# Kernel tuning notes

Measured on AMD Instinct MI355X. Metric: run time of the kernel, lower is better.

The kernel has to match this reference:

```python
import jax, jax.numpy as jnp
import numpy as np

IN, HID, B = 512, 512, 16384

def _linear_params(key, fan_in, fan_out, bias_const=None):
    kw, kb = jax.random.split(key)
    bound = 1.0 / np.sqrt(fan_in)
    W = jax.random.uniform(kw, (fan_out, fan_in), jnp.float32, -bound, bound)
    if bias_const is None:
        b = jax.random.uniform(kb, (fan_out,), jnp.float32, -bound, bound)
    else:
        b = jnp.full((fan_out,), bias_const, jnp.float32)
    return W, b

def setup_inputs() -> dict:
    key = jax.random.key(0)
    ks = jax.random.split(key, 11)
    x = jax.random.normal(ks[0], (B, IN), jnp.float32)
    h = jax.random.normal(ks[1], (B, HID), jnp.float32)
    c = jax.random.normal(ks[2], (B, HID), jnp.float32)
    Wxi, bxi = _linear_params(ks[3], IN, HID)
    Wxo, bxo = _linear_params(ks[4], IN, HID)
    Wxf, bxf = _linear_params(ks[5], IN, HID, bias_const=1.0)
    Wxg, bxg = _linear_params(ks[6], IN, HID)
    Whi, bhi = _linear_params(ks[7], HID, HID)
    Who, bho = _linear_params(ks[8], HID, HID)
    Whf, bhf = _linear_params(ks[9], HID, HID, bias_const=1.0)
    Whg, bhg = _linear_params(ks[10], HID, HID)
    return dict(x=x, h=h, c=c,
                Wxi=Wxi, bxi=bxi, Wxo=Wxo, bxo=bxo, Wxf=Wxf, bxf=bxf, Wxg=Wxg, bxg=bxg,
                Whi=Whi, bhi=bhi, Who=Who, bho=bho, Whf=Whf, bhf=bhf, Whg=Whg, bhg=bhg)

def reference(x, h, c,
              Wxi, bxi, Wxo, bxo, Wxf, bxf, Wxg, bxg,
              Whi, bhi, Who, bho, Whf, bhf, Whg, bhg):
    # Batch the four input projections and four hidden projections into two GEMMs.
    Wx = jnp.concatenate([Wxi, Wxg, Wxf, Wxo], axis=0)   # [4H, IN]
    Wh = jnp.concatenate([Whi, Whg, Whf, Who], axis=0)   # [4H, HID]
    bx = jnp.concatenate([bxi, bxg, bxf, bxo], axis=0)
    bh = jnp.concatenate([bhi, bhg, bhf, bho], axis=0)
    gates = x @ Wx.T + h @ Wh.T + bx + bh                 # [B, 4H]
    i_pre, g_pre, f_pre, o_pre = jnp.split(gates, 4, axis=1)
    i = jax.nn.sigmoid(i_pre)
    g = jnp.tanh(g_pre)
    f = jax.nn.sigmoid(f_pre)
    o = jax.nn.sigmoid(o_pre)
    c_new = f * c + i * g
    h_new = o * jnp.tanh(c_new)
    return (h_new, c_new)
```

## Files before the change

kernel.cpp:

```cpp
#include <hip/hip_runtime.h>
#include <cstdint>
#include <cstddef>


#define BATCH 16384
#define KDIM  1024
#define NPK   2048
#define HIDN  512

#define BM 256
#define BN 128
#define BK 32
#define NKT (KDIM / BK)

typedef __bf16 bf16x8 __attribute__((ext_vector_type(8)));
typedef float  f32x4  __attribute__((ext_vector_type(4)));

__device__ __forceinline__ unsigned short f2bf(float f) {
  unsigned int u = __builtin_bit_cast(unsigned int, f);
  u += 0x7fffu + ((u >> 16) & 1u);
  return (unsigned short)(u >> 16);
}

__device__ __forceinline__ float fast_sigmoid(float x) {
  return __builtin_amdgcn_rcpf(1.0f + __expf(-x));
}
__device__ __forceinline__ float fast_tanh(float x) {
  return 1.0f - 2.0f * __builtin_amdgcn_rcpf(1.0f + __expf(2.0f * x));
}

__device__ __forceinline__ void gload_lds16(const void* gp, void* lds_wave_base) {
  auto g = (const __attribute__((address_space(1))) unsigned int*)(unsigned long long)gp;
  auto l = (__attribute__((address_space(3))) unsigned int*)
           (unsigned int)(unsigned long long)lds_wave_base;
  __builtin_amdgcn_global_load_lds(g, l, 16, 0, 0);
}

__global__ __launch_bounds__(256) void pack_a(const float* __restrict__ x,
                                              const float* __restrict__ h,
                                              unsigned short* __restrict__ A) {
  int c = blockIdx.x * 256 + threadIdx.x;
  int idx = c << 3;
  int b = idx >> 10;
  int k = idx & 1023;
  const float* src = (k < 512) ? (x + (size_t)b * 512 + k)
                               : (h + (size_t)b * 512 + (k - 512));
  float4 lo = ((const float4*)src)[0];
  float4 hi = ((const float4*)src)[1];
  union { unsigned short s[8]; uint4 u; } o;
  o.s[0]=f2bf(lo.x); o.s[1]=f2bf(lo.y); o.s[2]=f2bf(lo.z); o.s[3]=f2bf(lo.w);
  o.s[4]=f2bf(hi.x); o.s[5]=f2bf(hi.y); o.s[6]=f2bf(hi.z); o.s[7]=f2bf(hi.w);
  ((uint4*)A)[c] = o.u;
}

struct GatePtrs {
  const float* wx[4];
  const float* wh[4];
  const float* bx[4];
  const float* bh[4];
};

__global__ __launch_bounds__(256) void pack_w(GatePtrs P,
                                              unsigned short* __restrict__ W,
                                              float* __restrict__ bias) {
  int c = blockIdx.x * 256 + threadIdx.x;
  int r = c >> 7;
  int k = (c & 127) << 3;
  int b    = r >> 7;
  int rem  = r & 127;
  int wn   = (rem >> 6) & 1;
  int gate = (rem >> 4) & 3;
  int jl   = rem & 15;
  int j = b * 32 + wn * 16 + jl;
  const float* src = (k < 512) ? (P.wx[gate] + (size_t)j * 512 + k)
                               : (P.wh[gate] + (size_t)j * 512 + (k - 512));
  float4 lo = ((const float4*)src)[0];
  float4 hi = ((const float4*)src)[1];
  union { unsigned short s[8]; uint4 u; } o;
  o.s[0]=f2bf(lo.x); o.s[1]=f2bf(lo.y); o.s[2]=f2bf(lo.z); o.s[3]=f2bf(lo.w);
  o.s[4]=f2bf(hi.x); o.s[5]=f2bf(hi.y); o.s[6]=f2bf(hi.z); o.s[7]=f2bf(hi.w);
  ((uint4*)W)[c] = o.u;
  if ((c & 127) == 0) bias[r] = P.bx[gate][j] + P.bh[gate][j];
}


__global__ __launch_bounds__(512, 4) void lstm_gemm(
    const unsigned short* __restrict__ A,
    const unsigned short* __restrict__ W,
    const float* __restrict__ bias,
    const float* __restrict__ Cin,
    float* __restrict__ Hout,
    float* __restrict__ Cout) {
  __shared__ __align__(16) unsigned short lds_a[2][BM * BK];
  __shared__ __align__(16) unsigned short lds_b[2][BN * BK];

  const int tid  = threadIdx.x;
  const int lane = tid & 63;
  const int wv   = tid >> 6;
  const int wm   = wv >> 1;
  const int wn   = wv & 1;

  const int lin = blockIdx.x;
  const int xcd = lin & 7;
  const int idx = lin >> 3;
  const int bn  = idx & 15;
  const int bm  = (idx >> 4) * 8 + xcd;

  const int srow = lane >> 2;
  const int scol = (lane & 3) << 3;
  const unsigned short* gA0 =
      A + (size_t)(bm * 256 + wv * 32 + srow) * KDIM + scol;
  const unsigned short* gA1 = gA0 + (size_t)16 * KDIM;
  const unsigned short* gB0 =
      W + (size_t)(bn * 128 + wv * 16 + srow) * KDIM + scol;
  const int laA0 = (wv * 32) * BK;
  const int laA1 = (wv * 32 + 16) * BK;
  const int laB  = (wv * 16) * BK;

  f32x4 acc[4][4] = {};

  const int lrow = lane & 15;
  const int kg   = (lane >> 4) << 3;

  gload_lds16(gA0, &lds_a[0][laA0]);
  gload_lds16(gA1, &lds_a[0][laA1]);
  gload_lds16(gB0, &lds_b[0][laB]);
  gA0 += BK; gA1 += BK; gB0 += BK;

  for (int kt = 0; kt < NKT; ++kt) {
    const int cur = kt & 1;
    __syncthreads();
    if (kt < NKT - 1) {
      gload_lds16(gA0, &lds_a[cur ^ 1][laA0]);
      gload_lds16(gA1, &lds_a[cur ^ 1][laA1]);
      gload_lds16(gB0, &lds_b[cur ^ 1][laB]);
      gA0 += BK; gA1 += BK; gB0 += BK;
    }

    bf16x8 af[4], bf[4];
#pragma unroll
    for (int mi = 0; mi < 4; ++mi)
      af[mi] = *reinterpret_cast<const bf16x8*>(
          &lds_a[cur][(wm * 64 + mi * 16 + lrow) * BK + kg]);
#pragma unroll
    for (int ni = 0; ni < 4; ++ni)
      bf[ni] = *reinterpret_cast<const bf16x8*>(
          &lds_b[cur][(wn * 64 + ni * 16 + lrow) * BK + kg]);
#pragma unroll
    for (int mi = 0; mi < 4; ++mi)
#pragma unroll
      for (int ni = 0; ni < 4; ++ni)
        acc[mi][ni] = __builtin_amdgcn_mfma_f32_16x16x32_bf16(
            af[mi], bf[ni], acc[mi][ni], 0, 0, 0);
  }

  const int jl = lane & 15;
  const int j  = bn * 32 + wn * 16 + jl;
  const int rbase = bm * 256 + wm * 64 + ((lane >> 4) << 2);
  float bv[4];
#pragma unroll
  for (int ni = 0; ni < 4; ++ni)
    bv[ni] = bias[bn * 128 + wn * 64 + ni * 16 + jl];

#pragma unroll
  for (int mi = 0; mi < 4; ++mi) {
#pragma unroll
    for (int r = 0; r < 4; ++r) {
      int row = rbase + mi * 16 + r;
      float iv = fast_sigmoid(acc[mi][0][r] + bv[0]);
      float gv = fast_tanh   (acc[mi][1][r] + bv[1]);
      float fv = fast_sigmoid(acc[mi][2][r] + bv[2]);
      float ov = fast_sigmoid(acc[mi][3][r] + bv[3]);
      float cold = Cin[(size_t)row * HIDN + j];
      float cnew = fv * cold + iv * gv;
      Hout[(size_t)row * HIDN + j] = ov * fast_tanh(cnew);
      Cout[(size_t)row * HIDN + j] = cnew;
    }
  }
}


extern "C" void kernel_launch(void* const* d_in, const int* in_sizes, int n_in,
                              void* d_out, int out_size, void* d_ws, size_t ws_size,
                              hipStream_t stream) {
  const float* x   = (const float*)d_in[0];
  const float* h   = (const float*)d_in[1];
  const float* c   = (const float*)d_in[2];
  const float* Wxi = (const float*)d_in[3];  const float* bxi = (const float*)d_in[4];
  const float* Wxo = (const float*)d_in[5];  const float* bxo = (const float*)d_in[6];
  const float* Wxf = (const float*)d_in[7];  const float* bxf = (const float*)d_in[8];
  const float* Wxg = (const float*)d_in[9];  const float* bxg = (const float*)d_in[10];
  const float* Whi = (const float*)d_in[11]; const float* bhi = (const float*)d_in[12];
  const float* Who = (const float*)d_in[13]; const float* bho = (const float*)d_in[14];
  const float* Whf = (const float*)d_in[15]; const float* bhf = (const float*)d_in[16];
  const float* Whg = (const float*)d_in[17]; const float* bhg = (const float*)d_in[18];

  char* ws = (char*)d_ws;
  unsigned short* Apack = (unsigned short*)ws;
  unsigned short* Wpack = (unsigned short*)(ws + (size_t)BATCH * KDIM * 2);
  float* biasp = (float*)(ws + (size_t)BATCH * KDIM * 2 + (size_t)NPK * KDIM * 2);

  pack_a<<<(BATCH * KDIM / 8) / 256, 256, 0, stream>>>(x, h, Apack);

  GatePtrs P;
  P.wx[0] = Wxi; P.wx[1] = Wxg; P.wx[2] = Wxf; P.wx[3] = Wxo;
  P.wh[0] = Whi; P.wh[1] = Whg; P.wh[2] = Whf; P.wh[3] = Who;
  P.bx[0] = bxi; P.bx[1] = bxg; P.bx[2] = bxf; P.bx[3] = bxo;
  P.bh[0] = bhi; P.bh[1] = bhg; P.bh[2] = bhf; P.bh[3] = bho;
  pack_w<<<(NPK * KDIM / 8) / 256, 256, 0, stream>>>(P, Wpack, biasp);

  float* Hout = (float*)d_out;
  float* Cout = Hout + (size_t)BATCH * HIDN;
  lstm_gemm<<<dim3((BATCH / BM) * (NPK / BN)), 512, 0, stream>>>(
      Apack, Wpack, biasp, c, Hout, Cout);
}
```

Before: 256.3 us.

## Enlarge GEMM tile to 256x256x64 with 8-wave ping-pong LDS pipeline

Grows the output tile to 256x256 with BK=64 and 8 waves laid out 2x4, each wave holding 128x64 of accumulators. A hand-scheduled loop stages global-to-LDS loads of the next tiles between MFMA blocks, using explicit barriers, waitcnts, sched_barriers and s_setprio so wave groups alternate between memory and compute. The aim is more reuse per LDS byte and better overlap of loads with MFMA. In exchange occupancy drops to 2 blocks per CU, register pressure rises, and the fragile manual vmcnt accounting risks races.

```diff
diff --git a/kernel.cpp b/kernel.cpp
--- a/kernel.cpp
+++ b/kernel.cpp
@@ -9,9 +9,9 @@
 #define HIDN  512
 
 #define BM 256
-#define BN 128
-#define BK 32
-#define NKT (KDIM / BK)
+#define BN 256
+#define BK 64
+#define NT (KDIM / BK)
 
 typedef __bf16 bf16x8 __attribute__((ext_vector_type(8)));
 typedef float  f32x4  __attribute__((ext_vector_type(4)));
@@ -84,89 +84,131 @@
 }
 
 
-__global__ __launch_bounds__(512, 4) void lstm_gemm(
+__global__ __launch_bounds__(512, 2) void lstm_gemm(
     const unsigned short* __restrict__ A,
     const unsigned short* __restrict__ W,
     const float* __restrict__ bias,
     const float* __restrict__ Cin,
     float* __restrict__ Hout,
     float* __restrict__ Cout) {
-  __shared__ __align__(16) unsigned short lds_a[2][BM * BK];
-  __shared__ __align__(16) unsigned short lds_b[2][BN * BK];
+  __shared__ __align__(16) unsigned short lds[2 * 32768];
 
   const int tid  = threadIdx.x;
   const int lane = tid & 63;
   const int wv   = tid >> 6;
-  const int wm   = wv >> 1;
-  const int wn   = wv & 1;
+  const int wm   = wv >> 2;
+  const int wn   = wv & 3;
 
   const int lin = blockIdx.x;
   const int xcd = lin & 7;
   const int idx = lin >> 3;
-  const int bn  = idx & 15;
-  const int bm  = (idx >> 4) * 8 + xcd;
+  const int bn  = idx & 7;
+  const int bm  = (idx >> 3) * 8 + xcd;
 
   const int srow = lane >> 2;
   const int scol = (lane & 3) << 3;
-  const unsigned short* gA0 =
-      A + (size_t)(bm * 256 + wv * 32 + srow) * KDIM + scol;
-  const unsigned short* gA1 = gA0 + (size_t)16 * KDIM;
-  const unsigned short* gB0 =
-      W + (size_t)(bn * 128 + wv * 16 + srow) * KDIM + scol;
-  const int laA0 = (wv * 32) * BK;
-  const int laA1 = (wv * 32 + 16) * BK;
-  const int laB  = (wv * 16) * BK;
-
-  f32x4 acc[4][4] = {};
+  const unsigned short* gA = A + (size_t)(bm * 256 + wv * 32 + srow) * KDIM + scol;
+  const unsigned short* gB = W + (size_t)(bn * 256 + wv * 32 + srow) * KDIM + scol;
+  const int lA = wv * 1024;
+
+#define REG_A(b, c) ((b) * 32768 + (c) * 8192)
+#define REG_B(b, c) ((b) * 32768 + 16384 + (c) * 8192)
+
+#define STAGE_A(b, c, tt) do {                                      \
+    const unsigned short* s_ = gA + (tt) * 64 + (c) * 32;           \
+    gload_lds16(s_,            &lds[REG_A(b, c) + lA]);             \
+    gload_lds16(s_ + 16 * KDIM, &lds[REG_A(b, c) + lA + 512]);      \
+  } while (0)
+#define STAGE_B(b, c, tt) do {                                      \
+    const unsigned short* s_ = gB + (tt) * 64 + (c) * 32;           \
+    gload_lds16(s_,            &lds[REG_B(b, c) + lA]);             \
+    gload_lds16(s_ + 16 * KDIM, &lds[REG_B(b, c) + lA + 512]);      \
+  } while (0)
 
   const int lrow = lane & 15;
   const int kg   = (lane >> 4) << 3;
-
-  gload_lds16(gA0, &lds_a[0][laA0]);
-  gload_lds16(gA1, &lds_a[0][laA1]);
-  gload_lds16(gB0, &lds_b[0][laB]);
-  gA0 += BK; gA1 += BK; gB0 += BK;
-
-  for (int kt = 0; kt < NKT; ++kt) {
-    const int cur = kt & 1;
-    __syncthreads();
-    if (kt < NKT - 1) {
-      gload_lds16(gA0, &lds_a[cur ^ 1][laA0]);
-      gload_lds16(gA1, &lds_a[cur ^ 1][laA1]);
-      gload_lds16(gB0, &lds_b[cur ^ 1][laB]);
-      gA0 += BK; gA1 += BK; gB0 += BK;
-    }
-
-    bf16x8 af[4], bf[4];
-#pragma unroll
-    for (int mi = 0; mi < 4; ++mi)
-      af[mi] = *reinterpret_cast<const bf16x8*>(
-          &lds_a[cur][(wm * 64 + mi * 16 + lrow) * BK + kg]);
-#pragma unroll
-    for (int ni = 0; ni < 4; ++ni)
-      bf[ni] = *reinterpret_cast<const bf16x8*>(
-          &lds_b[cur][(wn * 64 + ni * 16 + lrow) * BK + kg]);
-#pragma unroll
-    for (int mi = 0; mi < 4; ++mi)
-#pragma unroll
-      for (int ni = 0; ni < 4; ++ni)
-        acc[mi][ni] = __builtin_amdgcn_mfma_f32_16x16x32_bf16(
-            af[mi], bf[ni], acc[mi][ni], 0, 0, 0);
+  const int aoff = wm * 4096 + lrow * 32 + kg;
+  const int boff = wn * 2048 + lrow * 32 + kg;
+
+  f32x4 acc[8][4] = {};
+  bf16x8 af[4], bfr[4];
+
+#define LOAD_AF(b, c, h) do {                                                  \
+    _Pragma("unroll")                                                          \
+    for (int mi = 0; mi < 4; ++mi)                                             \
+      af[mi] = *reinterpret_cast<const bf16x8*>(                               \
+          &lds[REG_A(b, c) + aoff + (h) * 2048 + mi * 512]);                   \
+  } while (0)
+#define LOAD_BF(b, c) do {                                                     \
+    _Pragma("unroll")                                                          \
+    for (int ni = 0; ni < 4; ++ni)                                             \
+      bfr[ni] = *reinterpret_cast<const bf16x8*>(                              \
+          &lds[REG_B(b, c) + boff + ni * 512]);                                \
+  } while (0)
+#define MFMA_BLK(h) do {                                                       \
+    __builtin_amdgcn_s_setprio(1);                                             \
+    _Pragma("unroll")                                                          \
+    for (int mi = 0; mi < 4; ++mi)                                             \
+      _Pragma("unroll")                                                        \
+      for (int ni = 0; ni < 4; ++ni)                                           \
+        acc[(h) * 4 + mi][ni] = __builtin_amdgcn_mfma_f32_16x16x32_bf16(       \
+            af[mi], bfr[ni], acc[(h) * 4 + mi][ni], 0, 0, 0);                  \
+    __builtin_amdgcn_s_setprio(0);                                             \
+  } while (0)
+
+#define BAR()  __builtin_amdgcn_s_barrier()
+#define SCB()  __builtin_amdgcn_sched_barrier(0)
+#define WAIT_LGKM0() do { asm volatile("s_waitcnt lgkmcnt(0)" ::: "memory"); SCB(); } while (0)
+
+  STAGE_B(0, 0, 0); STAGE_A(0, 0, 0); STAGE_B(0, 1, 0); STAGE_A(0, 1, 0);
+  STAGE_B(1, 0, 1); STAGE_A(1, 0, 1); STAGE_B(1, 1, 1);
+  asm volatile("s_waitcnt vmcnt(6)" ::: "memory");
+  BAR(); SCB();
+
+#pragma unroll 2
+  for (int t = 0; t < NT; ++t) {
+    const int cur = t & 1;
+    const int nxt = cur ^ 1;
+    const int t1 = (t + 1 < NT) ? t + 1 : NT - 1;
+    const int t2 = (t + 2 < NT) ? t + 2 : NT - 1;
+    LOAD_AF(cur, 0, 0); LOAD_BF(cur, 0);
+    STAGE_A(nxt, 1, t1);
+    BAR(); WAIT_LGKM0();
+    MFMA_BLK(0);
+    BAR(); SCB();
+    LOAD_AF(cur, 0, 1);
+    STAGE_B(cur, 0, t2);
+    BAR(); WAIT_LGKM0();
+    MFMA_BLK(1);
+    BAR(); SCB();
+    LOAD_AF(cur, 1, 0); LOAD_BF(cur, 1);
+    STAGE_A(cur, 0, t2);
+    BAR(); WAIT_LGKM0();
+    MFMA_BLK(0);
+    BAR(); SCB();
+    LOAD_AF(cur, 1, 1);
+    STAGE_B(cur, 1, t2);
+    BAR(); WAIT_LGKM0();
+    MFMA_BLK(1);
+    asm volatile("s_waitcnt vmcnt(6)" ::: "memory");
+    BAR(); SCB();
   }
+  asm volatile("s_waitcnt vmcnt(0)" ::: "memory");
 
   const int jl = lane & 15;
-  const int j  = bn * 32 + wn * 16 + jl;
-  const int rbase = bm * 256 + wm * 64 + ((lane >> 4) << 2);
+  const int rq = (lane >> 4) << 2;
+  const int j  = (bn * 2 + (wn >> 1)) * 32 + (wn & 1) * 16 + jl;
   float bv[4];
 #pragma unroll
   for (int ni = 0; ni < 4; ++ni)
-    bv[ni] = bias[bn * 128 + wn * 64 + ni * 16 + jl];
+    bv[ni] = bias[bn * 256 + wn * 64 + ni * 16 + jl];
 
 #pragma unroll
-  for (int mi = 0; mi < 4; ++mi) {
+  for (int mi = 0; mi < 8; ++mi) {
+    const int row0 = bm * 256 + wm * 128 + (mi >> 2) * 64 + (mi & 3) * 16 + rq;
 #pragma unroll
     for (int r = 0; r < 4; ++r) {
-      int row = rbase + mi * 16 + r;
+      int row = row0 + r;
       float iv = fast_sigmoid(acc[mi][0][r] + bv[0]);
       float gv = fast_tanh   (acc[mi][1][r] + bv[1]);
       float fv = fast_sigmoid(acc[mi][2][r] + bv[2]);
```

Result: faster. 250.7 us (-2.2%).

## Pre-swizzle operands into MFMA fragment layout and load directly to registers

Applied to the files above, without the earlier changes.

Pack kernels now write A and W in a fragment-major layout matching 16x16x32 MFMA operand order, so the GEMM loads each fragment with one coalesced dwordx4 straight into VGPRs and skips LDS and barriers entirely. The GEMM tile grows to 256x256 with 4 waves each holding an 8x8 accumulator block, double-buffered in registers with explicit vmcnt waits and sched barriers. This removes LDS traffic and __syncthreads, but uses a very large register footprint (occupancy 1), and each wave reloads operands from global/L2 with no sharing across waves through LDS.

```diff
diff --git a/kernel.cpp b/kernel.cpp
--- a/kernel.cpp
+++ b/kernel.cpp
@@ -9,9 +9,8 @@
 #define HIDN  512
 
 #define BM 256
-#define BN 128
-#define BK 32
-#define NKT (KDIM / BK)
+#define BN 256
+#define NPH 32
 
 typedef __bf16 bf16x8 __attribute__((ext_vector_type(8)));
 typedef float  f32x4  __attribute__((ext_vector_type(4)));
@@ -29,28 +28,30 @@
   return 1.0f - 2.0f * __builtin_amdgcn_rcpf(1.0f + __expf(2.0f * x));
 }
 
-__device__ __forceinline__ void gload_lds16(const void* gp, void* lds_wave_base) {
-  auto g = (const __attribute__((address_space(1))) unsigned int*)(unsigned long long)gp;
-  auto l = (__attribute__((address_space(3))) unsigned int*)
-           (unsigned int)(unsigned long long)lds_wave_base;
-  __builtin_amdgcn_global_load_lds(g, l, 16, 0, 0);
-}
 
 __global__ __launch_bounds__(256) void pack_a(const float* __restrict__ x,
                                               const float* __restrict__ h,
                                               unsigned short* __restrict__ A) {
   int c = blockIdx.x * 256 + threadIdx.x;
-  int idx = c << 3;
-  int b = idx >> 10;
-  int k = idx & 1023;
-  const float* src = (k < 512) ? (x + (size_t)b * 512 + k)
-                               : (h + (size_t)b * 512 + (k - 512));
-  float4 lo = ((const float4*)src)[0];
-  float4 hi = ((const float4*)src)[1];
-  union { unsigned short s[8]; uint4 u; } o;
-  o.s[0]=f2bf(lo.x); o.s[1]=f2bf(lo.y); o.s[2]=f2bf(lo.z); o.s[3]=f2bf(lo.w);
-  o.s[4]=f2bf(hi.x); o.s[5]=f2bf(hi.y); o.s[6]=f2bf(hi.z); o.s[7]=f2bf(hi.w);
-  ((uint4*)A)[c] = o.u;
+  int rr4 = c & 3;
+  int ks  = (c >> 2) & 3;
+  int fk  = (c >> 4) & 31;
+  int fr  = c >> 9;
+  int k0  = fk * 32 + ks * 8;
+  const float* base = (k0 < 512) ? x : h;
+  int kk = (k0 < 512) ? k0 : k0 - 512;
+  unsigned short* out = A + ((size_t)fr * 32 + fk) * 512 + (ks * 16 + rr4 * 4) * 8;
+#pragma unroll
+  for (int i = 0; i < 4; ++i) {
+    int row = fr * 16 + rr4 * 4 + i;
+    const float* src = base + (size_t)row * 512 + kk;
+    float4 lo = ((const float4*)src)[0];
+    float4 hi = ((const float4*)src)[1];
+    union { unsigned short s[8]; uint4 u; } o;
+    o.s[0]=f2bf(lo.x); o.s[1]=f2bf(lo.y); o.s[2]=f2bf(lo.z); o.s[3]=f2bf(lo.w);
+    o.s[4]=f2bf(hi.x); o.s[5]=f2bf(hi.y); o.s[6]=f2bf(hi.z); o.s[7]=f2bf(hi.w);
+    ((uint4*)(out + i * 8))[0] = o.u;
+  }
 }
 
 struct GatePtrs {
@@ -64,36 +65,67 @@
                                               unsigned short* __restrict__ W,
                                               float* __restrict__ bias) {
   int c = blockIdx.x * 256 + threadIdx.x;
-  int r = c >> 7;
-  int k = (c & 127) << 3;
-  int b    = r >> 7;
-  int rem  = r & 127;
-  int wn   = (rem >> 6) & 1;
-  int gate = (rem >> 4) & 3;
-  int jl   = rem & 15;
-  int j = b * 32 + wn * 16 + jl;
-  const float* src = (k < 512) ? (P.wx[gate] + (size_t)j * 512 + k)
-                               : (P.wh[gate] + (size_t)j * 512 + (k - 512));
-  float4 lo = ((const float4*)src)[0];
-  float4 hi = ((const float4*)src)[1];
-  union { unsigned short s[8]; uint4 u; } o;
-  o.s[0]=f2bf(lo.x); o.s[1]=f2bf(lo.y); o.s[2]=f2bf(lo.z); o.s[3]=f2bf(lo.w);
-  o.s[4]=f2bf(hi.x); o.s[5]=f2bf(hi.y); o.s[6]=f2bf(hi.z); o.s[7]=f2bf(hi.w);
-  ((uint4*)W)[c] = o.u;
-  if ((c & 127) == 0) bias[r] = P.bx[gate][j] + P.bh[gate][j];
-}
-
-
-__global__ __launch_bounds__(512, 4) void lstm_gemm(
+  int rr4 = c & 3;
+  int ks  = (c >> 2) & 3;
+  int fk  = (c >> 4) & 31;
+  int fr  = c >> 9;
+  int k0  = fk * 32 + ks * 8;
+  int kk = (k0 < 512) ? k0 : k0 - 512;
+  unsigned short* out = W + ((size_t)fr * 32 + fk) * 512 + (ks * 16 + rr4 * 4) * 8;
+#pragma unroll
+  for (int i = 0; i < 4; ++i) {
+    int r = fr * 16 + rr4 * 4 + i;
+    int b    = r >> 7;
+    int rem  = r & 127;
+    int w64  = (rem >> 6) & 1;
+    int gate = (rem >> 4) & 3;
+    int jl   = rem & 15;
+    int j = b * 32 + w64 * 16 + jl;
+    const float* src = ((k0 < 512) ? P.wx[gate] : P.wh[gate]) + (size_t)j * 512 + kk;
+    float4 lo = ((const float4*)src)[0];
+    float4 hi = ((const float4*)src)[1];
+    union { unsigned short s[8]; uint4 u; } o;
+    o.s[0]=f2bf(lo.x); o.s[1]=f2bf(lo.y); o.s[2]=f2bf(lo.z); o.s[3]=f2bf(lo.w);
+    o.s[4]=f2bf(hi.x); o.s[5]=f2bf(hi.y); o.s[6]=f2bf(hi.z); o.s[7]=f2bf(hi.w);
+    ((uint4*)(out + i * 8))[0] = o.u;
+    if (fk == 0 && ks == 0) bias[r] = P.bx[gate][j] + P.bh[gate][j];
+  }
+}
+
+
+#define GLOAD(dst, voff, sptr)                                               \
+  asm volatile("global_load_dwordx4 %0, %1, %2"                              \
+               : "=v"(dst) : "v"(voff), "s"(sptr))
+
+#define ISSUE_PHASE(aset, bset, pA, pB) do {                                 \
+    GLOAD(aset[0], voffA[0], pA); GLOAD(aset[1], voffA[1], pA);              \
+    GLOAD(aset[2], voffA[2], pA); GLOAD(aset[3], voffA[3], pA);              \
+    GLOAD(aset[4], voffA[4], pA); GLOAD(aset[5], voffA[5], pA);              \
+    GLOAD(aset[6], voffA[6], pA); GLOAD(aset[7], voffA[7], pA);              \
+    GLOAD(bset[0], voffB[0], pB); GLOAD(bset[1], voffB[1], pB);              \
+    GLOAD(bset[2], voffB[2], pB); GLOAD(bset[3], voffB[3], pB);              \
+    GLOAD(bset[4], voffB[4], pB); GLOAD(bset[5], voffB[5], pB);              \
+    GLOAD(bset[6], voffB[6], pB); GLOAD(bset[7], voffB[7], pB);              \
+  } while (0)
+
+#define MFMA64(aset, bset) do {                                              \
+    _Pragma("unroll")                                                        \
+    for (int mi = 0; mi < 8; ++mi)                                           \
+      _Pragma("unroll")                                                      \
+      for (int ni = 0; ni < 8; ++ni)                                         \
+        acc[mi][ni] = __builtin_amdgcn_mfma_f32_16x16x32_bf16(               \
+            aset[mi], bset[ni], acc[mi][ni], 0, 0, 0);                       \
+  } while (0)
+
+#define SCB() __builtin_amdgcn_sched_barrier(0)
+
+__global__ __launch_bounds__(256, 1) void lstm_gemm(
     const unsigned short* __restrict__ A,
     const unsigned short* __restrict__ W,
     const float* __restrict__ bias,
     const float* __restrict__ Cin,
     float* __restrict__ Hout,
     float* __restrict__ Cout) {
-  __shared__ __align__(16) unsigned short lds_a[2][BM * BK];
-  __shared__ __align__(16) unsigned short lds_b[2][BN * BK];
-
   const int tid  = threadIdx.x;
   const int lane = tid & 63;
   const int wv   = tid >> 6;
@@ -103,78 +135,71 @@
   const int lin = blockIdx.x;
   const int xcd = lin & 7;
   const int idx = lin >> 3;
-  const int bn  = idx & 15;
-  const int bm  = (idx >> 4) * 8 + xcd;
-
-  const int srow = lane >> 2;
-  const int scol = (lane & 3) << 3;
-  const unsigned short* gA0 =
-      A + (size_t)(bm * 256 + wv * 32 + srow) * KDIM + scol;
-  const unsigned short* gA1 = gA0 + (size_t)16 * KDIM;
-  const unsigned short* gB0 =
-      W + (size_t)(bn * 128 + wv * 16 + srow) * KDIM + scol;
-  const int laA0 = (wv * 32) * BK;
-  const int laA1 = (wv * 32 + 16) * BK;
-  const int laB  = (wv * 16) * BK;
-
-  f32x4 acc[4][4] = {};
-
-  const int lrow = lane & 15;
-  const int kg   = (lane >> 4) << 3;
-
-  gload_lds16(gA0, &lds_a[0][laA0]);
-  gload_lds16(gA1, &lds_a[0][laA1]);
-  gload_lds16(gB0, &lds_b[0][laB]);
-  gA0 += BK; gA1 += BK; gB0 += BK;
-
-  for (int kt = 0; kt < NKT; ++kt) {
-    const int cur = kt & 1;
-    __syncthreads();
-    if (kt < NKT - 1) {
-      gload_lds16(gA0, &lds_a[cur ^ 1][laA0]);
-      gload_lds16(gA1, &lds_a[cur ^ 1][laA1]);
-      gload_lds16(gB0, &lds_b[cur ^ 1][laB]);
-      gA0 += BK; gA1 += BK; gB0 += BK;
-    }
-
-    bf16x8 af[4], bf[4];
-#pragma unroll
-    for (int mi = 0; mi < 4; ++mi)
-      af[mi] = *reinterpret_cast<const bf16x8*>(
-          &lds_a[cur][(wm * 64 + mi * 16 + lrow) * BK + kg]);
-#pragma unroll
-    for (int ni = 0; ni < 4; ++ni)
-      bf[ni] = *reinterpret_cast<const bf16x8*>(
-          &lds_b[cur][(wn * 64 + ni * 16 + lrow) * BK + kg]);
-#pragma unroll
-    for (int mi = 0; mi < 4; ++mi)
-#pragma unroll
-      for (int ni = 0; ni < 4; ++ni)
-        acc[mi][ni] = __builtin_amdgcn_mfma_f32_16x16x32_bf16(
-            af[mi], bf[ni], acc[mi][ni], 0, 0, 0);
-  }
+  const int bn  = idx & 7;
+  const int bm  = (idx >> 3) * 8 + xcd;
+
+  unsigned int voffA[8], voffB[8];
+#pragma unroll
+  for (int mi = 0; mi < 8; ++mi)
+    voffA[mi] = (unsigned int)((wm * 8 + mi) * 32768 + lane * 16);
+#pragma unroll
+  for (int ni = 0; ni < 8; ++ni)
+    voffB[ni] = (unsigned int)((wn * 8 + ni) * 32768 + lane * 16);
+
+  const unsigned short* baseA = A + (size_t)bm * 512 * 512;
+  const unsigned short* baseB = W + (size_t)bn * 512 * 512;
+
+  f32x4 acc[8][8] = {};
+  bf16x8 aX[8], bX[8];
+  bf16x8 aY[8], bY[8];
+
+  ISSUE_PHASE(aX, bX, baseA, baseB);
+  ISSUE_PHASE(aY, bY, baseA + 512, baseB + 512);
+
+#pragma unroll 1
+  for (int p = 0; p < NPH; p += 2) {
+    const int p2 = (p + 2 < NPH) ? p + 2 : NPH - 2;
+    const int p3 = (p + 3 < NPH) ? p + 3 : NPH - 1;
+    asm volatile("s_waitcnt vmcnt(16)" ::: "memory");
+    SCB();
+    MFMA64(aX, bX);
+    SCB();
+    ISSUE_PHASE(aX, bX, baseA + (size_t)p2 * 512, baseB + (size_t)p2 * 512);
+    asm volatile("s_waitcnt vmcnt(16)" ::: "memory");
+    SCB();
+    MFMA64(aY, bY);
+    SCB();
+    ISSUE_PHASE(aY, bY, baseA + (size_t)p3 * 512, baseB + (size_t)p3 * 512);
+  }
+  asm volatile("s_waitcnt vmcnt(0)" ::: "memory");
+  SCB();
 
   const int jl = lane & 15;
-  const int j  = bn * 32 + wn * 16 + jl;
-  const int rbase = bm * 256 + wm * 64 + ((lane >> 4) << 2);
-  float bv[4];
-#pragma unroll
-  for (int ni = 0; ni < 4; ++ni)
-    bv[ni] = bias[bn * 128 + wn * 64 + ni * 16 + jl];
-
-#pragma unroll
-  for (int mi = 0; mi < 4; ++mi) {
-#pragma unroll
-    for (int r = 0; r < 4; ++r) {
-      int row = rbase + mi * 16 + r;
-      float iv = fast_sigmoid(acc[mi][0][r] + bv[0]);
-      float gv = fast_tanh   (acc[mi][1][r] + bv[1]);
-      float fv = fast_sigmoid(acc[mi][2][r] + bv[2]);
-      float ov = fast_sigmoid(acc[mi][3][r] + bv[3]);
-      float cold = Cin[(size_t)row * HIDN + j];
-      float cnew = fv * cold + iv * gv;
-      Hout[(size_t)row * HIDN + j] = ov * fast_tanh(cnew);
-      Cout[(size_t)row * HIDN + j] = cnew;
+  const int rq = (lane >> 4) << 2;
+  const int bq = bn * 2 + wn;
+  float bv[8];
+#pragma unroll
+  for (int ni = 0; ni < 8; ++ni)
+    bv[ni] = bias[bq * 128 + (ni >> 2) * 64 + (ni & 3) * 16 + jl];
+
+#pragma unroll
+  for (int mi = 0; mi < 8; ++mi) {
+    const int row0 = bm * 256 + wm * 128 + mi * 16 + rq;
+#pragma unroll
+    for (int w64 = 0; w64 < 2; ++w64) {
+      const int j = bq * 32 + w64 * 16 + jl;
+#pragma unroll
+      for (int r = 0; r < 4; ++r) {
+        int row = row0 + r;
+        float iv = fast_sigmoid(acc[mi][w64 * 4 + 0][r] + bv[w64 * 4 + 0]);
+        float gv = fast_tanh   (acc[mi][w64 * 4 + 1][r] + bv[w64 * 4 + 1]);
+        float fv = fast_sigmoid(acc[mi][w64 * 4 + 2][r] + bv[w64 * 4 + 2]);
+        float ov = fast_sigmoid(acc[mi][w64 * 4 + 3][r] + bv[w64 * 4 + 3]);
+        float cold = Cin[(size_t)row * HIDN + j];
+        float cnew = fv * cold + iv * gv;
+        Hout[(size_t)row * HIDN + j] = ov * fast_tanh(cnew);
+        Cout[(size_t)row * HIDN + j] = cnew;
+      }
     }
   }
 }
@@ -200,17 +225,17 @@
   unsigned short* Wpack = (unsigned short*)(ws + (size_t)BATCH * KDIM * 2);
   float* biasp = (float*)(ws + (size_t)BATCH * KDIM * 2 + (size_t)NPK * KDIM * 2);
 
-  pack_a<<<(BATCH * KDIM / 8) / 256, 256, 0, stream>>>(x, h, Apack);
+  pack_a<<<(BATCH / 16) * 32 * 16 / 256, 256, 0, stream>>>(x, h, Apack);
 
   GatePtrs P;
   P.wx[0] = Wxi; P.wx[1] = Wxg; P.wx[2] = Wxf; P.wx[3] = Wxo;
   P.wh[0] = Whi; P.wh[1] = Whg; P.wh[2] = Whf; P.wh[3] = Who;
   P.bx[0] = bxi; P.bx[1] = bxg; P.bx[2] = bxf; P.bx[3] = bxo;
   P.bh[0] = bhi; P.bh[1] = bhg; P.bh[2] = bhf; P.bh[3] = bho;
-  pack_w<<<(NPK * KDIM / 8) / 256, 256, 0, stream>>>(P, Wpack, biasp);
+  pack_w<<<(NPK / 16) * 32 * 16 / 256, 256, 0, stream>>>(P, Wpack, biasp);
 
   float* Hout = (float*)d_out;
   float* Cout = Hout + (size_t)BATCH * HIDN;
-  lstm_gemm<<<dim3((BATCH / BM) * (NPK / BN)), 512, 0, stream>>>(
+  lstm_gemm<<<dim3((BATCH / BM) * (NPK / BN)), 256, 0, stream>>>(
       Apack, Wpack, biasp, c, Hout, Cout);
 }
```

Measured after the change: 427.5 us. 66.8% more time.
